# Kernel optimization log

Measured on AMD Instinct MI355X. Metric: run time of the kernel, lower is better.

The kernel has to match this reference:

```python
import jax, jax.numpy as jnp
import numpy as np

H = 150
PASSES = 5
NSETS = 2
N = 50000
E = 400000
G = 64
SLOPE = 0.01  # torch leaky_relu default


def setup_inputs() -> dict:
    key = jax.random.key(0)
    ks = jax.random.split(key, 20)
    def u(k, shape, fan):
        lim = 1.0 / np.sqrt(fan)
        return jax.random.uniform(k, shape, jnp.float32, -lim, lim)
    return {
        "nodes": jax.random.normal(ks[0], (N, H), jnp.float32),
        "problem_type": jax.random.uniform(ks[1], (G, 1), jnp.float32),
        "edge_W": u(ks[2], (NSETS, H, H), H),
        "edge_b": u(ks[3], (NSETS, H), H),
        "gru_w_ih": u(ks[4], (3 * H, H), H),
        "gru_w_hh": u(ks[5], (3 * H, H), H),
        "gru_b_ih": u(ks[6], (3 * H,), H),
        "gru_b_hh": u(ks[7], (3 * H,), H),
        "fc1_w": u(ks[8], (80, 151), 151),
        "fc1_b": u(ks[9], (80,), 151),
        "fc2_w": u(ks[10], (80, 80), 80),
        "fc2_b": u(ks[11], (80,), 80),
        "fcL_w": u(ks[12], (10, 80), 80),
        "fcL_b": u(ks[13], (10,), 80),
        "edges": jax.random.randint(ks[14], (NSETS, E, 2), 0, N),
        "graph_ids": jnp.sort(jax.random.randint(ks[15], (N,), 0, G)),
        "tbptt": 0,
    }


def _gru_cell(x, h, w_ih, w_hh, b_ih, b_hh):
    gi = x @ w_ih.T + b_ih  # [N, 3H]
    gh = h @ w_hh.T + b_hh
    ir, iz, inn = jnp.split(gi, 3, axis=-1)
    hr, hz, hn = jnp.split(gh, 3, axis=-1)
    r = jax.nn.sigmoid(ir + hr)
    z = jax.nn.sigmoid(iz + hz)
    n = jnp.tanh(inn + r * hn)
    return (1.0 - z) * n + z * h


def reference(nodes, problem_type, edge_W, edge_b, gru_w_ih, gru_w_hh,
              gru_b_ih, gru_b_hh, fc1_w, fc1_b, fc2_w, fc2_b, fcL_w, fcL_b,
              edges, graph_ids, tbptt):
    n_sets = edge_W.shape[0]
    n_graphs = problem_type.shape[0]
    for j in range(PASSES):
        incoming = jnp.zeros_like(nodes)
        for k in range(n_sets):
            src = edges[k, :, 1]
            dst = edges[k, :, 0]
            # NOTE: in the source, the first Linear+leaky_relu result is
            # overwritten; the effective edge message is just the second Linear.
            y = nodes[src] @ edge_W[k].T + edge_b[k]  # [E, H]
            incoming = incoming.at[dst].add(y)
        nodes = _gru_cell(incoming, nodes, gru_w_ih, gru_w_hh, gru_b_ih, gru_b_hh)
        if tbptt == 1 and j < PASSES - 2:
            nodes = jax.lax.stop_gradient(nodes)
    g = jax.ops.segment_sum(nodes, graph_ids, num_segments=n_graphs)  # [G, H]
    g = jnp.log(g)
    g = jnp.where(jnp.isnan(g), 0.0, g)
    g = jax.nn.relu(g)
    x = jnp.concatenate([g, problem_type], axis=1)  # [G, 151]
    x = jax.nn.leaky_relu(x @ fc1_w.T + fc1_b, SLOPE)
    x = jax.nn.leaky_relu(x @ fc2_w.T + fc2_b, SLOPE)
    return x @ fcL_w.T + fcL_b  # [G, 10]
```

## Files before the change

### kernel.cpp

```cpp
#include <hip/hip_runtime.h>
#include <stdint.h>

#define NN 50000
#define H 150
#define NE 400000
#define NG 64
#define NPASS 5
#define KB 480
#define VC 640
#define NRB 391

typedef unsigned short u16;
typedef unsigned int u32;
typedef __attribute__((ext_vector_type(8))) short short8;
typedef __attribute__((ext_vector_type(4))) float float4v;
typedef __attribute__((ext_vector_type(4))) u32 uint4v;
typedef __attribute__((ext_vector_type(2))) u32 uint2v;

__device__ __forceinline__ u16 f2bf_rn(float x) {
  union { float f; u32 u; } v; v.f = x;
  u32 r = v.u + 0x7fffu + ((v.u >> 16) & 1u);
  return (u16)(r >> 16);
}
__device__ __forceinline__ float bf2f(u16 h) {
  union { u32 u; float f; } v; v.u = ((u32)h) << 16;
  return v.f;
}
__device__ __forceinline__ u32 packf(float v) {
  u16 hi = f2bf_rn(v);
  u16 lo = f2bf_rn(v - bf2f(hi));
  return (u32)hi | ((u32)lo << 16);
}
__device__ __forceinline__ float upk(u32 u) {
  union { u32 u; float f; } a, b;
  a.u = u << 16; b.u = u & 0xffff0000u;
  return a.f + b.f;
}
__device__ __forceinline__ void async16(const void* g, void* l) {
  __builtin_amdgcn_global_load_lds(
      (const __attribute__((address_space(1))) unsigned int*)(uintptr_t)g,
      (__attribute__((address_space(3))) unsigned int*)(uint32_t)(uintptr_t)l,
      16, 0, 0);
}

__global__ void hist_kernel(const int* __restrict__ edges, int* __restrict__ cnt) {
  int id = blockIdx.x * 256 + threadIdx.x;
  if (id >= 2 * NE) return;
  int dst = edges[id * 2];
  int set = id / NE;
  atomicAdd(&cnt[dst * 2 + set], 1);
}

__global__ __launch_bounds__(1024) void scan1_kernel(const int* __restrict__ cnt,
                                                     int* __restrict__ rowptr,
                                                     int* __restrict__ bsum, int n) {
  __shared__ int sd[1024];
  int t = threadIdx.x;
  int idx = blockIdx.x * 1024 + t;
  int v = (idx < n) ? cnt[idx] : 0;
  sd[t] = v;
  __syncthreads();
  for (int off = 1; off < 1024; off <<= 1) {
    int add = (t >= off) ? sd[t - off] : 0;
    __syncthreads();
    sd[t] += add;
    __syncthreads();
  }
  if (idx < n) rowptr[idx] = sd[t] - v;
  if (t == 1023) bsum[blockIdx.x] = sd[1023];
}

__global__ __launch_bounds__(128) void scan2_kernel(const int* __restrict__ bsum,
                                                    int* __restrict__ boff, int nb) {
  __shared__ int sd[128];
  int t = threadIdx.x;
  int v = (t < nb) ? bsum[t] : 0;
  sd[t] = v;
  __syncthreads();
  for (int off = 1; off < 128; off <<= 1) {
    int add = (t >= off) ? sd[t - off] : 0;
    __syncthreads();
    sd[t] += add;
    __syncthreads();
  }
  boff[t] = sd[t] - v;
}

__global__ void scan3_kernel(int* __restrict__ rowptr, const int* __restrict__ boff, int n) {
  int idx = blockIdx.x * 256 + threadIdx.x;
  if (idx < n) rowptr[idx] += boff[idx >> 10];
}

__global__ void total_kernel(int* __restrict__ rowptr, const int* __restrict__ boff, int n, int nb) {
  if (threadIdx.x == 0 && blockIdx.x == 0) rowptr[n] = boff[nb];
}

__global__ void copy_int_kernel(const int* __restrict__ a, int* __restrict__ b, int n) {
  int id = blockIdx.x * 256 + threadIdx.x;
  if (id < n) b[id] = a[id];
}

__global__ void fill_kernel(const int* __restrict__ edges, int* __restrict__ cursor,
                            u16* __restrict__ colbuf) {
  int id = blockIdx.x * 256 + threadIdx.x;
  if (id >= 2 * NE) return;
  int dst = edges[id * 2];
  int src = edges[id * 2 + 1];
  int set = id / NE;
  int pos = atomicAdd(&cursor[dst * 2 + set], 1);
  colbuf[pos] = (u16)src;
}

__global__ void bounds_kernel(const int* __restrict__ gids, int* __restrict__ gstart) {
  int g = threadIdx.x;
  if (g > NG) return;
  int lo = 0, hi = NN;
  while (lo < hi) { int m = (lo + hi) >> 1; if (gids[m] < g) lo = m + 1; else hi = m; }
  gstart[g] = lo;
}

__global__ void build_B_kernel(const float* __restrict__ wih, const float* __restrict__ whh,
                               const float* __restrict__ eW,
                               u16* __restrict__ Bh, u16* __restrict__ Bl) {
  int id = blockIdx.x * 256 + threadIdx.x;
  if (id >= VC * KB) return;
  int v = id / KB, k = id % KB;
  int g = (v >> 4) & 3, c = (v >> 6) * 16 + (v & 15);
  int seg = k / 160, kk = k % 160;
  float val = 0.f;
  if (c < H && kk < H) {
    if (seg < 2) {
      if (g < 3) {
        const float* wr = wih + (size_t)(g * H + c) * H;
        const float* wc = eW + (size_t)seg * H * H + kk;
        float acc = 0.f;
        for (int t = 0; t < H; t++) acc += wr[t] * wc[(size_t)t * H];
        val = acc;
      }
    } else {
      if (g == 0) val = whh[(size_t)c * H + kk];
      else if (g == 1) val = whh[(size_t)(H + c) * H + kk];
      else if (g == 3) val = whh[(size_t)(2 * H + c) * H + kk];
    }
  }
  u16 h = f2bf_rn(val);
  Bh[id] = h;
  Bl[id] = f2bf_rn(val - bf2f(h));
}

__global__ void build_coef_kernel(const float* __restrict__ wih,
                                  const float* __restrict__ eb,
                                  const float* __restrict__ bih, const float* __restrict__ bhh,
                                  float* __restrict__ coefs) {
  int id = threadIdx.x + blockIdx.x * 256;
  if (id >= VC) return;
  int g = id / 160, c = id % 160;
  float u0 = 0.f, u1 = 0.f, bs = 0.f;
  if (c < H) {
    if (g < 3) {
      const float* wr = wih + (size_t)(g * H + c) * H;
      for (int t = 0; t < H; t++) { u0 += wr[t] * eb[t]; u1 += wr[t] * eb[H + t]; }
    }
    if (g == 0) bs = bih[c] + bhh[c];
    else if (g == 1) bs = bih[H + c] + bhh[H + c];
    else if (g == 2) bs = bih[2 * H + c];
    else bs = bhh[2 * H + c];
  }
  coefs[id] = u0;
  coefs[VC + id] = u1;
  coefs[2 * VC + id] = bs;
}

__global__ void init_nodes_kernel(const float* __restrict__ nin,
                                  u32* __restrict__ npkA, u32* __restrict__ npkB) {
  int id = blockIdx.x * 256 + threadIdx.x;
  if (id >= NN * 160) return;
  int r = id / 160, c = id % 160;
  if (c < H) {
    npkA[id] = packf(nin[(size_t)r * H + c]);
  } else {
    npkA[id] = 0;
    npkB[id] = 0;
  }
}

__global__ void pad_S_kernel(u32* __restrict__ Snp) {
  int id = blockIdx.x * 256 + threadIdx.x;
  if (id >= NN * 20) return;
  int r = id / 20, rem = id % 20;
  int set = rem / 10, t = rem % 10;
  Snp[(size_t)r * 320 + set * 160 + H + t] = 0;
}

__global__ __launch_bounds__(256) void gather_kernel(
    const u32* __restrict__ npk, const int* __restrict__ rowptr,
    const u16* __restrict__ colbuf, u32* __restrict__ Snp) {
  int gtid = blockIdx.x * 256 + threadIdx.x;
  int wid = gtid >> 6;
  if (wid >= 2 * NN) return;
  int node = wid >> 1, set = wid & 1;
  int lane = gtid & 63;
  int s = rowptr[2 * node + set], e = rowptr[2 * node + set + 1];
  int deg = e - s;
  int cA = 2 * lane, cC = 128 + lane;
  bool okC = (cC < H);
  float aA = 0.f, aB = 0.f, aC = 0.f;
  for (int base = 0; base < deg; base += 64) {
    int rem = min(64, deg - base);
    u32 srcv = 0;
    if (lane < rem) srcv = (u32)colbuf[s + base + lane];
    int i = 0;
    for (; i + 3 < rem; i += 4) {
      u32 r0 = (u32)__builtin_amdgcn_readlane((int)srcv, i);
      u32 r1 = (u32)__builtin_amdgcn_readlane((int)srcv, i + 1);
      u32 r2 = (u32)__builtin_amdgcn_readlane((int)srcv, i + 2);
      u32 r3 = (u32)__builtin_amdgcn_readlane((int)srcv, i + 3);
      const u32* p0 = npk + (size_t)r0 * 160;
      const u32* p1 = npk + (size_t)r1 * 160;
      const u32* p2 = npk + (size_t)r2 * 160;
      const u32* p3 = npk + (size_t)r3 * 160;
      uint2v v0 = *(const uint2v*)(p0 + cA);
      uint2v v1 = *(const uint2v*)(p1 + cA);
      uint2v v2 = *(const uint2v*)(p2 + cA);
      uint2v v3 = *(const uint2v*)(p3 + cA);
      u32 w0 = 0, w1 = 0, w2 = 0, w3 = 0;
      if (okC) { w0 = p0[cC]; w1 = p1[cC]; w2 = p2[cC]; w3 = p3[cC]; }
      aA += upk(v0.x) + upk(v1.x);
      aB += upk(v0.y) + upk(v1.y);
      if (okC) aC += upk(w0) + upk(w1);
      aA += upk(v2.x) + upk(v3.x);
      aB += upk(v2.y) + upk(v3.y);
      if (okC) aC += upk(w2) + upk(w3);
    }
    for (; i + 1 < rem; i += 2) {
      u32 r0 = (u32)__builtin_amdgcn_readlane((int)srcv, i);
      u32 r1 = (u32)__builtin_amdgcn_readlane((int)srcv, i + 1);
      const u32* p0 = npk + (size_t)r0 * 160;
      const u32* p1 = npk + (size_t)r1 * 160;
      uint2v v0 = *(const uint2v*)(p0 + cA);
      uint2v v1 = *(const uint2v*)(p1 + cA);
      aA += upk(v0.x) + upk(v1.x);
      aB += upk(v0.y) + upk(v1.y);
      if (okC) aC += upk(p0[cC]) + upk(p1[cC]);
    }
    if (i < rem) {
      u32 r0 = (u32)__builtin_amdgcn_readlane((int)srcv, i);
      const u32* p0 = npk + (size_t)r0 * 160;
      uint2v v0 = *(const uint2v*)(p0 + cA);
      aA += upk(v0.x);
      aB += upk(v0.y);
      if (okC) aC += upk(p0[cC]);
    }
  }
  u32* o = Snp + (size_t)node * 320 + set * 160;
  o[cA] = packf(aA);
  o[cA + 1] = packf(aB);
  if (okC) o[cC] = packf(aC);
}


template<int KT>
__device__ __forceinline__ void stage_fn(
    const u32* __restrict__ Snp, const u32* __restrict__ npkc,
    const u16* __restrict__ Bhp, const u16* __restrict__ Blp,
    char* Ab, char* Bb, int tid, int w, int r0, int ccb) {
  #pragma unroll
  for (int i = 0; i < 4; i++) {
    int cl = i * 256 + tid;
    int row = cl >> 3;
    int q = (cl & 7) ^ (row & 7);
    int rg = min(r0 + row, NN - 1);
    if constexpr (KT < 10)
      async16(Snp + (size_t)rg * 320 + KT * 32 + q * 4, Ab + i * 4096 + w * 1024);
    else
      async16(npkc + (size_t)rg * 160 + (KT - 10) * 32 + q * 4, Ab + i * 4096 + w * 1024);
  }
  constexpr int koffB = (KT < 10) ? KT * 32 : 320 + (KT - 10) * 32;
  constexpr int skipg = (KT < 10) ? 3 : 2;
  #pragma unroll
  for (int i = 0; i < 2; i++) {
    int cl = i * 256 + tid;
    int row = cl >> 2;
    int q = (cl & 3) ^ ((row >> 1) & 3);
    if (((row >> 4) & 3) != skipg) {
      size_t gb = (size_t)(ccb * 128 + row) * KB + koffB + q * 8;
      int lb = i * 4096 + w * 1024;
      async16(Bhp + gb, Bb + lb);
      async16(Blp + gb, Bb + 8192 + lb);
    }
  }
}

template<int KTn>
__device__ __forceinline__ void read_frags_fn(
    const char* Ab, const char* Bb, int m, int quad, int mrow0, int nco0,
    uint4v (&A0)[4], uint4v (&A1)[4], short8 (&RBh)[3], short8 (&RBl)[3]) {
  #pragma unroll
  for (int jj = 0; jj < 3; jj++) {
    const int jsel = (jj == 2) ? ((KTn < 10) ? 2 : 3) : jj;
    int br = nco0 + jsel * 16 + m;
    int bd = br * 64 + ((quad ^ ((br >> 1) & 3)) * 16);
    RBh[jj] = *(const short8*)(Bb + bd);
    RBl[jj] = *(const short8*)(Bb + 8192 + bd);
  }
  #pragma unroll
  for (int mt = 0; mt < 4; mt++) {
    int r = mrow0 + mt * 16 + m;
    A0[mt] = *(const uint4v*)(Ab + r * 128 + (((2 * quad) ^ (r & 7)) * 16));
    A1[mt] = *(const uint4v*)(Ab + r * 128 + (((2 * quad + 1) ^ (r & 7)) * 16));
  }
}

template<int KT>
__device__ __forceinline__ void mfma_fn(
    const uint4v (&A0)[4], const uint4v (&A1)[4],
    const short8 (&MBh)[3], const short8 (&MBl)[3], float4v (&acc)[4][4]) {
  #pragma unroll
  for (int mt = 0; mt < 4; mt++) {
    u32 uu[8] = {A0[mt].x, A0[mt].y, A0[mt].z, A0[mt].w,
                 A1[mt].x, A1[mt].y, A1[mt].z, A1[mt].w};
    short8 ah, al;
    #pragma unroll
    for (int e2 = 0; e2 < 8; e2++) {
      ah[e2] = (short)(uu[e2] & 0xffffu);
      al[e2] = (short)(uu[e2] >> 16);
    }
    #pragma unroll
    for (int jj = 0; jj < 3; jj++) {
      const int J = (KT < 10) ? jj : ((jj == 2) ? 3 : jj);
      acc[mt][J] = __builtin_amdgcn_mfma_f32_16x16x32_bf16(ah, MBh[jj], acc[mt][J], 0, 0, 0);
      acc[mt][J] = __builtin_amdgcn_mfma_f32_16x16x32_bf16(ah, MBl[jj], acc[mt][J], 0, 0, 0);
      acc[mt][J] = __builtin_amdgcn_mfma_f32_16x16x32_bf16(al, MBh[jj], acc[mt][J], 0, 0, 0);
    }
  }
}

template<int KT>
__device__ __forceinline__ void gemm_step(
    const u32* __restrict__ Snp, const u32* __restrict__ npkc,
    const u16* __restrict__ Bhp, const u16* __restrict__ Blp,
    char (&Abuf)[2][16384], char (&Bbuf)[2][16384],
    int tid, int w, int m, int quad, int mrow0, int nco0, int r0, int ccb,
    uint4v (&A0)[2][4], uint4v (&A1)[2][4], short8 (&FBh)[2][3], short8 (&FBl)[2][3],
    float4v (&acc)[4][4]) {
  constexpr int cur = KT & 1;
  constexpr int nxt = cur ^ 1;
  if constexpr (KT + 2 <= 14)
    stage_fn<KT + 2>(Snp, npkc, Bhp, Blp, Abuf[cur], Bbuf[cur], tid, w, r0, ccb);
  if constexpr (KT + 1 <= 14) {
    if constexpr (KT + 2 <= 14) {
      constexpr int lw = (KT + 2 < 10) ? 3 : 2;
      if (w == lw) { asm volatile("s_waitcnt vmcnt(4)" ::: "memory"); }
      else         { asm volatile("s_waitcnt vmcnt(8)" ::: "memory"); }
    } else {
      asm volatile("s_waitcnt vmcnt(0)" ::: "memory");
    }
    __builtin_amdgcn_sched_barrier(0);
    __builtin_amdgcn_s_barrier();
    read_frags_fn<KT + 1>(Abuf[nxt], Bbuf[nxt], m, quad, mrow0, nco0,
                          A0[nxt], A1[nxt], FBh[nxt], FBl[nxt]);
    __builtin_amdgcn_sched_barrier(0);
  }
  __builtin_amdgcn_s_setprio(1);
  mfma_fn<KT>(A0[cur], A1[cur], FBh[cur], FBl[cur], acc);
  __builtin_amdgcn_s_setprio(0);
  if constexpr (KT + 3 <= 14) {
    asm volatile("s_waitcnt lgkmcnt(0)" ::: "memory");
    __builtin_amdgcn_sched_barrier(0);
    __builtin_amdgcn_s_barrier();
  }
}

__global__ __launch_bounds__(256) void gru_gemm_kernel(
    const u32* __restrict__ Snp, const u32* __restrict__ npkc,
    const u16* __restrict__ Bhp, const u16* __restrict__ Blp,
    const float* __restrict__ coefs, const int* __restrict__ rowptr,
    u32* __restrict__ npkn) {
  __shared__ char Abuf[2][16384];
  __shared__ char Bbuf[2][16384];
  const int bid = blockIdx.x;
  const int xcd = bid & 7;
  const int rest = bid >> 3;
  const int ccb = rest % 5;
  const int r0b = (rest / 5) * 8 + xcd;
  if (r0b >= NRB) return;
  const int r0 = r0b * 128;
  const int tid = threadIdx.x;
  const int w = tid >> 6, l = tid & 63;
  const int m = l & 15, quad = l >> 4;
  const int mrow0 = (w & 1) * 64;
  const int nco0 = (w >> 1) * 64;

  float4v acc[4][4];
  #pragma unroll
  for (int mt = 0; mt < 4; mt++)
    #pragma unroll
    for (int j = 0; j < 4; j++) acc[mt][j] = (float4v){0.f, 0.f, 0.f, 0.f};

  uint4v A0[2][4], A1[2][4];
  short8 FBh[2][3], FBl[2][3];

  stage_fn<0>(Snp, npkc, Bhp, Blp, Abuf[0], Bbuf[0], tid, w, r0, ccb);
  stage_fn<1>(Snp, npkc, Bhp, Blp, Abuf[1], Bbuf[1], tid, w, r0, ccb);
  if (w == 3) { asm volatile("s_waitcnt vmcnt(4)" ::: "memory"); }
  else        { asm volatile("s_waitcnt vmcnt(8)" ::: "memory"); }
  __builtin_amdgcn_sched_barrier(0);
  __builtin_amdgcn_s_barrier();
  read_frags_fn<0>(Abuf[0], Bbuf[0], m, quad, mrow0, nco0,
                   A0[0], A1[0], FBh[0], FBl[0]);
  asm volatile("s_waitcnt lgkmcnt(0)" ::: "memory");
  __builtin_amdgcn_sched_barrier(0);
  __builtin_amdgcn_s_barrier();

  #define STEP(K) gemm_step<K>(Snp, npkc, Bhp, Blp, Abuf, Bbuf, tid, w, m, quad, \
                               mrow0, nco0, r0, ccb, A0, A1, FBh, FBl, acc)
  STEP(0);  STEP(1);  STEP(2);  STEP(3);  STEP(4);
  STEP(5);  STEP(6);  STEP(7);  STEP(8);  STEP(9);
  STEP(10); STEP(11); STEP(12); STEP(13); STEP(14);
  #undef STEP

  int c = (ccb * 2 + (w >> 1)) * 16 + m;
  if (c >= H) return;
  float u0r = coefs[c],            u0z = coefs[160 + c],
        u0n = coefs[320 + c];
  float u1r = coefs[VC + c],       u1z = coefs[VC + 160 + c],
        u1n = coefs[VC + 320 + c];
  float bsr = coefs[2 * VC + c],   bsz = coefs[2 * VC + 160 + c],
        bsn = coefs[2 * VC + 320 + c], bsh = coefs[2 * VC + 480 + c];
  #pragma unroll
  for (int mt = 0; mt < 4; mt++) {
    #pragma unroll
    for (int i = 0; i < 4; i++) {
      int row = r0 + mrow0 + mt * 16 + quad * 4 + i;
      if (row >= NN) continue;
      float d0 = (float)(rowptr[2 * row + 1] - rowptr[2 * row]);
      float d1 = (float)(rowptr[2 * row + 2] - rowptr[2 * row + 1]);
      float pr = acc[mt][0][i] + d0 * u0r + d1 * u1r + bsr;
      float pz = acc[mt][1][i] + d0 * u0z + d1 * u1z + bsz;
      float pn = acc[mt][2][i] + d0 * u0n + d1 * u1n + bsn;
      float ph = acc[mt][3][i] + bsh;
      float r_g = 1.f / (1.f + __expf(-pr));
      float z_g = 1.f / (1.f + __expf(-pz));
      float narg = pn + r_g * ph;
      float e2 = __expf(2.f * narg);
      float n_g = 1.f - 2.f / (e2 + 1.f);
      float h = upk(npkc[(size_t)row * 160 + c]);
      npkn[(size_t)row * 160 + c] = packf((1.f - z_g) * n_g + z_g * h);
    }
  }
}

__global__ __launch_bounds__(192) void segsum_kernel(const u32* __restrict__ npk,
                                                     const int* __restrict__ gstart,
                                                     float* __restrict__ gsum) {
  int g = blockIdx.x, chunk = blockIdx.y;
  int c = threadIdx.x;
  if (c >= H) return;
  int s = gstart[g], e = gstart[g + 1];
  int len = e - s;
  if (len <= 0) return;
  int per = (len + 3) / 4;
  int rs = s + chunk * per;
  int re = min(e, rs + per);
  if (rs >= re) return;
  float acc = 0.f;
  for (int r = rs; r < re; r++) acc += upk(npk[(size_t)r * 160 + c]);
  atomicAdd(&gsum[g * H + c], acc);
}

__global__ __launch_bounds__(192) void head_kernel(
    const float* __restrict__ gsum, const float* __restrict__ pt,
    const float* __restrict__ fc1_w, const float* __restrict__ fc1_b,
    const float* __restrict__ fc2_w, const float* __restrict__ fc2_b,
    const float* __restrict__ fcL_w, const float* __restrict__ fcL_b,
    float* __restrict__ out) {
  __shared__ float x[151];
  __shared__ float x1[80];
  __shared__ float x2[80];
  int row = blockIdx.x;
  int t = threadIdx.x;
  if (t < 151) {
    float v;
    if (t < H) { float g = gsum[row * H + t]; v = (g > 1.f) ? logf(g) : 0.f; }
    else v = pt[row];
    x[t] = v;
  }
  __syncthreads();
  if (t < 80) {
    float acc = fc1_b[t];
    const float* wrow = fc1_w + t * 151;
    #pragma unroll 4
    for (int k = 0; k < 151; k++) acc += x[k] * wrow[k];
    x1[t] = (acc > 0.f) ? acc : 0.01f * acc;
  }
  __syncthreads();
  if (t < 80) {
    float acc = fc2_b[t];
    const float* wrow = fc2_w + t * 80;
    #pragma unroll 4
    for (int k = 0; k < 80; k++) acc += x1[k] * wrow[k];
    x2[t] = (acc > 0.f) ? acc : 0.01f * acc;
  }
  __syncthreads();
  if (t < 10) {
    float acc = fcL_b[t];
    const float* wrow = fcL_w + t * 80;
    #pragma unroll 4
    for (int k = 0; k < 80; k++) acc += x2[k] * wrow[k];
    out[row * 10 + t] = acc;
  }
}

extern "C" void kernel_launch(void* const* d_in, const int* in_sizes, int n_in,
                              void* d_out, int out_size, void* d_ws, size_t ws_size,
                              hipStream_t stream) {
  const float* nodes_in = (const float*)d_in[0];
  const float* problem_type = (const float*)d_in[1];
  const float* edge_W = (const float*)d_in[2];
  const float* edge_b = (const float*)d_in[3];
  const float* w_ih = (const float*)d_in[4];
  const float* w_hh = (const float*)d_in[5];
  const float* b_ih = (const float*)d_in[6];
  const float* b_hh = (const float*)d_in[7];
  const float* fc1_w = (const float*)d_in[8];
  const float* fc1_b = (const float*)d_in[9];
  const float* fc2_w = (const float*)d_in[10];
  const float* fc2_b = (const float*)d_in[11];
  const float* fcL_w = (const float*)d_in[12];
  const float* fcL_b = (const float*)d_in[13];
  const int* edges = (const int*)d_in[14];
  const int* graph_ids = (const int*)d_in[15];

  char* ws = (char*)d_ws;
  size_t off = 0;
  auto alloc = [&](size_t bytes) -> void* {
    void* p = ws + off;
    off = (off + bytes + 255) & ~(size_t)255;
    return p;
  };
  u32* npkA     = (u32*)alloc((size_t)NN * 160 * 4);
  u32* npkB     = (u32*)alloc((size_t)NN * 160 * 4);
  u32* Snp      = (u32*)alloc((size_t)NN * 320 * 4);
  u16* Bh       = (u16*)alloc((size_t)VC * KB * 2);
  u16* Bl       = (u16*)alloc((size_t)VC * KB * 2);
  float* coefs  = (float*)alloc(3 * VC * 4);
  int* rowptr   = (int*)alloc((2 * NN + 1) * 4);
  int* cursor   = (int*)alloc(2 * NN * 4);
  u16* colbuf   = (u16*)alloc(2ull * NE * 2);
  int* bsum     = (int*)alloc(128 * 4);
  int* boff     = (int*)alloc(128 * 4);
  int* gstart   = (int*)alloc((NG + 1) * 4);
  float* gsum   = (float*)alloc((size_t)NG * H * 4);

  const int n2 = 2 * NN;
  const int nb = (n2 + 1023) / 1024;

  hipMemsetAsync(cursor, 0, n2 * 4, stream);
  hist_kernel<<<(2 * NE + 255) / 256, 256, 0, stream>>>(edges, cursor);
  scan1_kernel<<<nb, 1024, 0, stream>>>(cursor, rowptr, bsum, n2);
  scan2_kernel<<<1, 128, 0, stream>>>(bsum, boff, nb);
  scan3_kernel<<<(n2 + 255) / 256, 256, 0, stream>>>(rowptr, boff, n2);
  total_kernel<<<1, 64, 0, stream>>>(rowptr, boff, n2, nb);
  copy_int_kernel<<<(n2 + 255) / 256, 256, 0, stream>>>(rowptr, cursor, n2);
  fill_kernel<<<(2 * NE + 255) / 256, 256, 0, stream>>>(edges, cursor, colbuf);
  bounds_kernel<<<1, 128, 0, stream>>>(graph_ids, gstart);
  build_B_kernel<<<(VC * KB + 255) / 256, 256, 0, stream>>>(w_ih, w_hh, edge_W, Bh, Bl);
  build_coef_kernel<<<(VC + 255) / 256, 256, 0, stream>>>(w_ih, edge_b, b_ih, b_hh, coefs);
  init_nodes_kernel<<<(NN * 160 + 255) / 256, 256, 0, stream>>>(nodes_in, npkA, npkB);
  pad_S_kernel<<<(NN * 20 + 255) / 256, 256, 0, stream>>>(Snp);

  const int ngrp = (NRB + 7) / 8;
  u32* nbuf[2] = {npkA, npkB};
  for (int pass = 0; pass < NPASS; pass++) {
    u32* cur = nbuf[pass & 1];
    u32* nxt = nbuf[1 - (pass & 1)];
    gather_kernel<<<(2 * NN * 64 + 255) / 256, 256, 0, stream>>>(cur, rowptr, colbuf, Snp);
    gru_gemm_kernel<<<ngrp * 5 * 8, 256, 0, stream>>>(
        Snp, cur, Bh, Bl, coefs, rowptr, nxt);
  }
  u32* fin = nbuf[NPASS & 1];

  hipMemsetAsync(gsum, 0, (size_t)NG * H * 4, stream);
  segsum_kernel<<<dim3(NG, 4), 192, 0, stream>>>(fin, gstart, gsum);
  head_kernel<<<NG, 192, 0, stream>>>(gsum, problem_type, fc1_w, fc1_b, fc2_w, fc2_b,
                                      fcL_w, fcL_b, (float*)d_out);
}
```

Before: 1.137 ms.

## Load GRU GEMM fragments directly from global memory into registers, dropping LDS staging

The GRU GEMM kernel previously staged A and B tiles through double-buffered shared memory using async global-to-LDS loads, with barriers every k-step. It now has each lane load its MFMA fragments straight from global memory into a register double buffer, prefetching two steps ahead and using vmcnt waits without any workgroup barriers. Launch bounds now request two blocks per CU. This removes LDS traffic and barrier stalls, but loses the sharing of loaded tiles across waves, so B and A data are fetched redundantly per wave and rely on cache hits. Register pressure also rises under the new occupancy hint.

```diff
diff --git a/kernel.cpp b/kernel.cpp
--- a/kernel.cpp
+++ b/kernel.cpp
@@ -35,12 +35,6 @@
   union { u32 u; float f; } a, b;
   a.u = u << 16; b.u = u & 0xffff0000u;
   return a.f + b.f;
-}
-__device__ __forceinline__ void async16(const void* g, void* l) {
-  __builtin_amdgcn_global_load_lds(
-      (const __attribute__((address_space(1))) unsigned int*)(uintptr_t)g,
-      (__attribute__((address_space(3))) unsigned int*)(uint32_t)(uintptr_t)l,
-      16, 0, 0);
 }
 
 __global__ void hist_kernel(const int* __restrict__ edges, int* __restrict__ cnt) {
@@ -260,58 +254,6 @@
 
 
 template<int KT>
-__device__ __forceinline__ void stage_fn(
-    const u32* __restrict__ Snp, const u32* __restrict__ npkc,
-    const u16* __restrict__ Bhp, const u16* __restrict__ Blp,
-    char* Ab, char* Bb, int tid, int w, int r0, int ccb) {
-  #pragma unroll
-  for (int i = 0; i < 4; i++) {
-    int cl = i * 256 + tid;
-    int row = cl >> 3;
-    int q = (cl & 7) ^ (row & 7);
-    int rg = min(r0 + row, NN - 1);
-    if constexpr (KT < 10)
-      async16(Snp + (size_t)rg * 320 + KT * 32 + q * 4, Ab + i * 4096 + w * 1024);
-    else
-      async16(npkc + (size_t)rg * 160 + (KT - 10) * 32 + q * 4, Ab + i * 4096 + w * 1024);
-  }
-  constexpr int koffB = (KT < 10) ? KT * 32 : 320 + (KT - 10) * 32;
-  constexpr int skipg = (KT < 10) ? 3 : 2;
-  #pragma unroll
-  for (int i = 0; i < 2; i++) {
-    int cl = i * 256 + tid;
-    int row = cl >> 2;
-    int q = (cl & 3) ^ ((row >> 1) & 3);
-    if (((row >> 4) & 3) != skipg) {
-      size_t gb = (size_t)(ccb * 128 + row) * KB + koffB + q * 8;
-      int lb = i * 4096 + w * 1024;
-      async16(Bhp + gb, Bb + lb);
-      async16(Blp + gb, Bb + 8192 + lb);
-    }
-  }
-}
-
-template<int KTn>
-__device__ __forceinline__ void read_frags_fn(
-    const char* Ab, const char* Bb, int m, int quad, int mrow0, int nco0,
-    uint4v (&A0)[4], uint4v (&A1)[4], short8 (&RBh)[3], short8 (&RBl)[3]) {
-  #pragma unroll
-  for (int jj = 0; jj < 3; jj++) {
-    const int jsel = (jj == 2) ? ((KTn < 10) ? 2 : 3) : jj;
-    int br = nco0 + jsel * 16 + m;
-    int bd = br * 64 + ((quad ^ ((br >> 1) & 3)) * 16);
-    RBh[jj] = *(const short8*)(Bb + bd);
-    RBl[jj] = *(const short8*)(Bb + 8192 + bd);
-  }
-  #pragma unroll
-  for (int mt = 0; mt < 4; mt++) {
-    int r = mrow0 + mt * 16 + m;
-    A0[mt] = *(const uint4v*)(Ab + r * 128 + (((2 * quad) ^ (r & 7)) * 16));
-    A1[mt] = *(const uint4v*)(Ab + r * 128 + (((2 * quad + 1) ^ (r & 7)) * 16));
-  }
-}
-
-template<int KT>
 __device__ __forceinline__ void mfma_fn(
     const uint4v (&A0)[4], const uint4v (&A1)[4],
     const short8 (&MBh)[3], const short8 (&MBl)[3], float4v (&acc)[4][4]) {
@@ -335,49 +277,57 @@
   }
 }
 
+template<int KT, int BUF>
+__device__ __forceinline__ void load_frags(
+    const u32* const (&aS)[4], const u32* const (&aN)[4],
+    const u16* __restrict__ Bhp, const u16* __restrict__ Blp,
+    const u32 (&bo1)[3], const u32 (&bo2)[3],
+    uint4v (&A0)[2][4], uint4v (&A1)[2][4],
+    short8 (&FBh)[2][3], short8 (&FBl)[2][3]) {
+  if constexpr (KT <= 14) {
+    #pragma unroll
+    for (int mt = 0; mt < 4; mt++) {
+      const u32* p = (KT < 10) ? (aS[mt] + KT * 32) : (aN[mt] + (KT - 10) * 32);
+      A0[BUF][mt] = *(const uint4v*)p;
+      A1[BUF][mt] = *(const uint4v*)(p + 4);
+    }
+    constexpr int koffB = (KT < 10) ? KT * 32 : 320 + (KT - 10) * 32;
+    #pragma unroll
+    for (int jj = 0; jj < 3; jj++) {
+      u32 off = ((KT < 10) ? bo1[jj] : bo2[jj]) + koffB;
+      FBh[BUF][jj] = *(const short8*)(Bhp + off);
+      FBl[BUF][jj] = *(const short8*)(Blp + off);
+    }
+  }
+}
+
 template<int KT>
 __device__ __forceinline__ void gemm_step(
-    const u32* __restrict__ Snp, const u32* __restrict__ npkc,
+    const u32* const (&aS)[4], const u32* const (&aN)[4],
     const u16* __restrict__ Bhp, const u16* __restrict__ Blp,
-    char (&Abuf)[2][16384], char (&Bbuf)[2][16384],
-    int tid, int w, int m, int quad, int mrow0, int nco0, int r0, int ccb,
-    uint4v (&A0)[2][4], uint4v (&A1)[2][4], short8 (&FBh)[2][3], short8 (&FBl)[2][3],
-    float4v (&acc)[4][4]) {
+    const u32 (&bo1)[3], const u32 (&bo2)[3],
+    uint4v (&A0)[2][4], uint4v (&A1)[2][4],
+    short8 (&FBh)[2][3], short8 (&FBl)[2][3], float4v (&acc)[4][4]) {
   constexpr int cur = KT & 1;
-  constexpr int nxt = cur ^ 1;
-  if constexpr (KT + 2 <= 14)
-    stage_fn<KT + 2>(Snp, npkc, Bhp, Blp, Abuf[cur], Bbuf[cur], tid, w, r0, ccb);
   if constexpr (KT + 1 <= 14) {
-    if constexpr (KT + 2 <= 14) {
-      constexpr int lw = (KT + 2 < 10) ? 3 : 2;
-      if (w == lw) { asm volatile("s_waitcnt vmcnt(4)" ::: "memory"); }
-      else         { asm volatile("s_waitcnt vmcnt(8)" ::: "memory"); }
-    } else {
-      asm volatile("s_waitcnt vmcnt(0)" ::: "memory");
-    }
-    __builtin_amdgcn_sched_barrier(0);
-    __builtin_amdgcn_s_barrier();
-    read_frags_fn<KT + 1>(Abuf[nxt], Bbuf[nxt], m, quad, mrow0, nco0,
-                          A0[nxt], A1[nxt], FBh[nxt], FBl[nxt]);
-    __builtin_amdgcn_sched_barrier(0);
-  }
+    asm volatile("s_waitcnt vmcnt(14)" ::: "memory");
+  } else {
+    asm volatile("s_waitcnt vmcnt(0)" ::: "memory");
+  }
+  __builtin_amdgcn_sched_barrier(0);
   __builtin_amdgcn_s_setprio(1);
   mfma_fn<KT>(A0[cur], A1[cur], FBh[cur], FBl[cur], acc);
   __builtin_amdgcn_s_setprio(0);
-  if constexpr (KT + 3 <= 14) {
-    asm volatile("s_waitcnt lgkmcnt(0)" ::: "memory");
-    __builtin_amdgcn_sched_barrier(0);
-    __builtin_amdgcn_s_barrier();
-  }
-}
-
-__global__ __launch_bounds__(256) void gru_gemm_kernel(
+  __builtin_amdgcn_sched_barrier(0);
+  load_frags<KT + 2, cur>(aS, aN, Bhp, Blp, bo1, bo2, A0, A1, FBh, FBl);
+  __builtin_amdgcn_sched_barrier(0);
+}
+
+__global__ __launch_bounds__(256, 2) void gru_gemm_kernel(
     const u32* __restrict__ Snp, const u32* __restrict__ npkc,
     const u16* __restrict__ Bhp, const u16* __restrict__ Blp,
     const float* __restrict__ coefs, const int* __restrict__ rowptr,
     u32* __restrict__ npkn) {
-  __shared__ char Abuf[2][16384];
-  __shared__ char Bbuf[2][16384];
   const int bid = blockIdx.x;
   const int xcd = bid & 7;
   const int rest = bid >> 3;
@@ -391,6 +341,26 @@
   const int mrow0 = (w & 1) * 64;
   const int nco0 = (w >> 1) * 64;
 
+  const u32* aS[4];
+  const u32* aN[4];
+  #pragma unroll
+  for (int mt = 0; mt < 4; mt++) {
+    int rg = min(r0 + mrow0 + mt * 16 + m, NN - 1);
+    aS[mt] = Snp + (size_t)rg * 320 + quad * 8;
+    aN[mt] = npkc + (size_t)rg * 160 + quad * 8;
+  }
+  u32 bo1[3], bo2[3];
+  {
+    const int bc = ccb * 128 + nco0;
+    #pragma unroll
+    for (int jj = 0; jj < 3; jj++) {
+      const int js1 = jj;
+      const int js2 = (jj == 2) ? 3 : jj;
+      bo1[jj] = (u32)(bc + js1 * 16 + m) * KB + quad * 8;
+      bo2[jj] = (u32)(bc + js2 * 16 + m) * KB + quad * 8;
+    }
+  }
+
   float4v acc[4][4];
   #pragma unroll
   for (int mt = 0; mt < 4; mt++)
@@ -400,20 +370,12 @@
   uint4v A0[2][4], A1[2][4];
   short8 FBh[2][3], FBl[2][3];
 
-  stage_fn<0>(Snp, npkc, Bhp, Blp, Abuf[0], Bbuf[0], tid, w, r0, ccb);
-  stage_fn<1>(Snp, npkc, Bhp, Blp, Abuf[1], Bbuf[1], tid, w, r0, ccb);
-  if (w == 3) { asm volatile("s_waitcnt vmcnt(4)" ::: "memory"); }
-  else        { asm volatile("s_waitcnt vmcnt(8)" ::: "memory"); }
+  load_frags<0, 0>(aS, aN, Bhp, Blp, bo1, bo2, A0, A1, FBh, FBl);
   __builtin_amdgcn_sched_barrier(0);
-  __builtin_amdgcn_s_barrier();
-  read_frags_fn<0>(Abuf[0], Bbuf[0], m, quad, mrow0, nco0,
-                   A0[0], A1[0], FBh[0], FBl[0]);
-  asm volatile("s_waitcnt lgkmcnt(0)" ::: "memory");
+  load_frags<1, 1>(aS, aN, Bhp, Blp, bo1, bo2, A0, A1, FBh, FBl);
   __builtin_amdgcn_sched_barrier(0);
-  __builtin_amdgcn_s_barrier();
-
-  #define STEP(K) gemm_step<K>(Snp, npkc, Bhp, Blp, Abuf, Bbuf, tid, w, m, quad, \
-                               mrow0, nco0, r0, ccb, A0, A1, FBh, FBl, acc)
+
+  #define STEP(K) gemm_step<K>(aS, aN, Bhp, Blp, bo1, bo2, A0, A1, FBh, FBl, acc)
   STEP(0);  STEP(1);  STEP(2);  STEP(3);  STEP(4);
   STEP(5);  STEP(6);  STEP(7);  STEP(8);  STEP(9);
   STEP(10); STEP(11); STEP(12); STEP(13); STEP(14);
```

New measurement: 1.494 ms. 1.31x slower.

## Replace double-buffered GRU GEMM pipeline with single buffer for higher occupancy

Applied to the files above, without the earlier changes.

Switches the GRU GEMM kernel from a two-stage LDS double buffer with register-prefetched fragments to a single LDS buffer. Each step now reads fragments, then issues the next tile's global loads, runs the MFMAs, and waits for the loads to finish. Halving LDS and fragment registers, together with a launch bound of 4 blocks per CU, aims to raise occupancy so other waves hide latency. The cost is less intra-wave overlap and a full vmcnt(0) wait plus barrier every step.

```diff
diff --git a/kernel.cpp b/kernel.cpp
--- a/kernel.cpp
+++ b/kernel.cpp
@@ -339,45 +339,36 @@
 __device__ __forceinline__ void gemm_step(
     const u32* __restrict__ Snp, const u32* __restrict__ npkc,
     const u16* __restrict__ Bhp, const u16* __restrict__ Blp,
-    char (&Abuf)[2][16384], char (&Bbuf)[2][16384],
+    char (&Abuf)[16384], char (&Bbuf)[16384],
     int tid, int w, int m, int quad, int mrow0, int nco0, int r0, int ccb,
-    uint4v (&A0)[2][4], uint4v (&A1)[2][4], short8 (&FBh)[2][3], short8 (&FBl)[2][3],
     float4v (&acc)[4][4]) {
-  constexpr int cur = KT & 1;
-  constexpr int nxt = cur ^ 1;
-  if constexpr (KT + 2 <= 14)
-    stage_fn<KT + 2>(Snp, npkc, Bhp, Blp, Abuf[cur], Bbuf[cur], tid, w, r0, ccb);
+  uint4v A0[4], A1[4];
+  short8 FBh[3], FBl[3];
+  read_frags_fn<KT>(Abuf, Bbuf, m, quad, mrow0, nco0, A0, A1, FBh, FBl);
+  asm volatile("s_waitcnt lgkmcnt(0)" ::: "memory");
+  __builtin_amdgcn_sched_barrier(0);
+  __builtin_amdgcn_s_barrier();
+  if constexpr (KT + 1 <= 14)
+    stage_fn<KT + 1>(Snp, npkc, Bhp, Blp, Abuf, Bbuf, tid, w, r0, ccb);
+  __builtin_amdgcn_sched_barrier(0);
+  __builtin_amdgcn_s_setprio(1);
+  mfma_fn<KT>(A0, A1, FBh, FBl, acc);
+  __builtin_amdgcn_s_setprio(0);
+  __builtin_amdgcn_sched_barrier(0);
   if constexpr (KT + 1 <= 14) {
-    if constexpr (KT + 2 <= 14) {
-      constexpr int lw = (KT + 2 < 10) ? 3 : 2;
-      if (w == lw) { asm volatile("s_waitcnt vmcnt(4)" ::: "memory"); }
-      else         { asm volatile("s_waitcnt vmcnt(8)" ::: "memory"); }
-    } else {
-      asm volatile("s_waitcnt vmcnt(0)" ::: "memory");
-    }
+    asm volatile("s_waitcnt vmcnt(0)" ::: "memory");
     __builtin_amdgcn_sched_barrier(0);
     __builtin_amdgcn_s_barrier();
-    read_frags_fn<KT + 1>(Abuf[nxt], Bbuf[nxt], m, quad, mrow0, nco0,
-                          A0[nxt], A1[nxt], FBh[nxt], FBl[nxt]);
-    __builtin_amdgcn_sched_barrier(0);
-  }
-  __builtin_amdgcn_s_setprio(1);
-  mfma_fn<KT>(A0[cur], A1[cur], FBh[cur], FBl[cur], acc);
-  __builtin_amdgcn_s_setprio(0);
-  if constexpr (KT + 3 <= 14) {
-    asm volatile("s_waitcnt lgkmcnt(0)" ::: "memory");
-    __builtin_amdgcn_sched_barrier(0);
-    __builtin_amdgcn_s_barrier();
-  }
-}
-
-__global__ __launch_bounds__(256) void gru_gemm_kernel(
+  }
+}
+
+__global__ __launch_bounds__(256, 4) void gru_gemm_kernel(
     const u32* __restrict__ Snp, const u32* __restrict__ npkc,
     const u16* __restrict__ Bhp, const u16* __restrict__ Blp,
     const float* __restrict__ coefs, const int* __restrict__ rowptr,
     u32* __restrict__ npkn) {
-  __shared__ char Abuf[2][16384];
-  __shared__ char Bbuf[2][16384];
+  __shared__ char Abuf[16384];
+  __shared__ char Bbuf[16384];
   const int bid = blockIdx.x;
   const int xcd = bid & 7;
   const int rest = bid >> 3;
@@ -397,23 +388,13 @@
     #pragma unroll
     for (int j = 0; j < 4; j++) acc[mt][j] = (float4v){0.f, 0.f, 0.f, 0.f};
 
-  uint4v A0[2][4], A1[2][4];
-  short8 FBh[2][3], FBl[2][3];
-
-  stage_fn<0>(Snp, npkc, Bhp, Blp, Abuf[0], Bbuf[0], tid, w, r0, ccb);
-  stage_fn<1>(Snp, npkc, Bhp, Blp, Abuf[1], Bbuf[1], tid, w, r0, ccb);
-  if (w == 3) { asm volatile("s_waitcnt vmcnt(4)" ::: "memory"); }
-  else        { asm volatile("s_waitcnt vmcnt(8)" ::: "memory"); }
+  stage_fn<0>(Snp, npkc, Bhp, Blp, Abuf, Bbuf, tid, w, r0, ccb);
+  asm volatile("s_waitcnt vmcnt(0)" ::: "memory");
   __builtin_amdgcn_sched_barrier(0);
   __builtin_amdgcn_s_barrier();
-  read_frags_fn<0>(Abuf[0], Bbuf[0], m, quad, mrow0, nco0,
-                   A0[0], A1[0], FBh[0], FBl[0]);
-  asm volatile("s_waitcnt lgkmcnt(0)" ::: "memory");
-  __builtin_amdgcn_sched_barrier(0);
-  __builtin_amdgcn_s_barrier();
 
   #define STEP(K) gemm_step<K>(Snp, npkc, Bhp, Blp, Abuf, Bbuf, tid, w, m, quad, \
-                               mrow0, nco0, r0, ccb, A0, A1, FBh, FBl, acc)
+                               mrow0, nco0, r0, ccb, acc)
   STEP(0);  STEP(1);  STEP(2);  STEP(3);  STEP(4);
   STEP(5);  STEP(6);  STEP(7);  STEP(8);  STEP(9);
   STEP(10); STEP(11); STEP(12); STEP(13); STEP(14);
```

Result: no change. 1.129 ms (-0.7%).
